# Kernel tuning notes

Measured on AMD Instinct MI355X. Metric: run time of the kernel, lower is better.

Reference implementation:

```python
import jax, jax.numpy as jnp
import numpy as np

B, N, M, C = 4, 4096, 4096, 256
IMG_W, IMG_H = 1280.0, 384.0


def setup_inputs() -> dict:
    key = jax.random.key(0)
    ks = jax.random.split(key, 12)
    nodes_L = jax.random.normal(ks[0], (B, N, C), dtype=jnp.float32)
    nodes_R = jax.random.normal(ks[1], (B, M, C), dtype=jnp.float32)
    # pixel coordinates: (u, v) with u in [0, IMG_W), v in [0, IMG_H)
    scale = jnp.array([IMG_W, IMG_H], dtype=jnp.float32)
    kpts_L = jax.random.uniform(ks[2], (B, N, 2), dtype=jnp.float32) * scale
    kpts_R = jax.random.uniform(ks[3], (B, M, 2), dtype=jnp.float32) * scale
    s = 1.0 / np.sqrt(C)
    Wq = jax.random.normal(ks[4], (C, C), dtype=jnp.float32) * s
    bq = jnp.zeros((C,), dtype=jnp.float32)
    Wk = jax.random.normal(ks[5], (C, C), dtype=jnp.float32) * s
    bk = jnp.zeros((C,), dtype=jnp.float32)
    Wv = jax.random.normal(ks[6], (C, C), dtype=jnp.float32) * s
    bv = jnp.zeros((C,), dtype=jnp.float32)
    Wm = jax.random.normal(ks[7], (C, C), dtype=jnp.float32) * s
    bm = jnp.zeros((C,), dtype=jnp.float32)
    return {"nodes_L": nodes_L, "nodes_R": nodes_R, "kpts_L": kpts_L, "kpts_R": kpts_R,
            "Wq": Wq, "bq": bq, "Wk": Wk, "bk": bk, "Wv": Wv, "bv": bv, "Wm": Wm, "bm": bm}


def reference(nodes_L, nodes_R, kpts_L, kpts_R, Wq, bq, Wk, bk, Wv, bv, Wm, bm):
    dim = nodes_L.shape[-1]
    # torch Linear: x @ W.T + b
    Q = nodes_L @ Wq.T + bq                      # [B,N,C]
    K = nodes_R @ Wk.T + bk                      # [B,M,C]
    V = nodes_R @ Wv.T + bv                      # [B,M,C]
    # epipolar geometry terms, [B,N,M]
    dist_v = jnp.abs(kpts_L[:, :, 1:2] - kpts_R[:, :, 1][:, None, :])
    dist_u = kpts_L[:, :, 0:1] - kpts_R[:, :, 0][:, None, :]
    mask = (dist_v < 3.0) & (dist_u > 0) & (dist_u < 192)
    attn = jnp.einsum('bnc,bmc->bnm', Q, K) / jnp.sqrt(jnp.float32(dim))
    attn = jnp.where(mask, attn, jnp.float32(-1e9))
    attn_weights = jax.nn.softmax(attn, axis=-1)  # [B,N,M]
    matched = jnp.einsum('bnm,bmc->bnc', attn_weights, V)
    init_disparity = jnp.sum(attn_weights * dist_u, axis=-1, keepdims=True)  # [B,N,1]
    confidence = jnp.any(mask, axis=-1, keepdims=True).astype(jnp.float32)   # [B,N,1]
    return matched @ Wm.T + bm, init_disparity, confidence
```

## Files before the change

### kernel.cpp

```cpp
#include <hip/hip_runtime.h>
#include <hip/hip_bf16.h>

#define BB 4
#define NN 4096
#define MM 4096
#define CC 256
#define CAP 128
#define NBIN 384
#define NCH 16
#define CHK 256

typedef __attribute__((ext_vector_type(8))) short bf16x8;
typedef __attribute__((ext_vector_type(4))) float f32x4;

static __device__ __forceinline__ float bf2f(unsigned short u) {
    return __uint_as_float(((unsigned)u) << 16);
}
static __device__ __forceinline__ unsigned short f2bf(float f) {
    unsigned u = __float_as_uint(f);
    u += 0x7fffu + ((u >> 16) & 1u);
    return (unsigned short)(u >> 16);
}
static __device__ __forceinline__ bf16x8 asbf(uint4 u) {
    union { uint4 a; bf16x8 b; } c; c.a = u; return c.b;
}
static __device__ __forceinline__ void gload16(const unsigned short* g, unsigned short* l) {
    __builtin_amdgcn_global_load_lds(
        (const __attribute__((address_space(1))) unsigned int*)g,
        (__attribute__((address_space(3))) unsigned int*)l, 16, 0, 0);
}

__global__ __launch_bounds__(256) void prep_kernel(
    const float* __restrict__ Wq, const float* __restrict__ Wk,
    const float* __restrict__ Wv, const float* __restrict__ Wm,
    const float* __restrict__ L, const float* __restrict__ R,
    const float* __restrict__ kptsR,
    unsigned short* __restrict__ Wpk, unsigned short* __restrict__ Lpk,
    unsigned short* __restrict__ Rpk,
    int* __restrict__ hist, unsigned short* __restrict__ prank,
    float* __restrict__ Vsum, float* __restrict__ Usum)
{
    __shared__ __align__(16) unsigned char SMEM[32768];
    const int tid = threadIdx.x, y = blockIdx.y, x = blockIdx.x;

    if (y < 4) {
        const float* S = (y == 0) ? Wq : (y == 1) ? Wk : (y == 2) ? Wv : Wm;
        int o = x * 256 + tid;
        int j = o & 7, lane = (o >> 3) & 63, kt = o >> 9;
        int kk = kt >> 4, t = kt & 15;
        int r = t * 16 + (lane & 15), c = kk * 32 + (lane >> 4) * 8 + j;
        Wpk[(size_t)y * 65536 + o] = f2bf(S[r * 256 + c]);
        return;
    }
    if (y < 6) {
        const float* S = (y == 5) ? R : L;
        unsigned short* D = (y == 5) ? Rpk : Lpk;
        unsigned short* T = (unsigned short*)SMEM;
        const int wid = tid >> 6, lane = tid & 63;
        const size_t R0 = (size_t)x * 64;
#pragma unroll
        for (int it = 0; it < 16; ++it) {
            int row = it * 4 + wid;
            float4 f = *(const float4*)(S + (R0 + row) * 256 + lane * 4);
            ushort4 h = make_ushort4(f2bf(f.x), f2bf(f.y), f2bf(f.z), f2bf(f.w));
            int col = lane * 4;
            *(ushort4*)&T[row * 256 + (col ^ ((row & 7) << 3))] = h;
        }
        __syncthreads();
        unsigned short* Dp = D + (size_t)x * 16384;
#pragma unroll
        for (int p = 0; p < 8; ++p) {
            int u = p * 2048 + tid * 8;
            int rt = u >> 12, rem = u & 4095;
            int kk = rem >> 9, ln = (rem >> 3) & 63;
            int row = rt * 16 + (ln & 15);
            int col = kk * 32 + (ln >> 4) * 8;
            *(uint4*)(Dp + u) = *(const uint4*)&T[row * 256 + (col ^ ((row & 7) << 3))];
        }
        return;
    }
    if (y == 6) {
        if (x >= NCH * BB) return;
        int chunk = x & 15, b = x >> 4;
        int* h = (int*)SMEM;
        short* sbin = (short*)(SMEM + NBIN * 4);
        for (int i = tid; i < NBIN; i += CHK) h[i] = 0;
        int m = chunk * CHK + tid;
        float2 p = ((const float2*)kptsR)[(size_t)b * MM + m];
        int bin = (int)p.y;
        sbin[tid] = (short)bin;
        __syncthreads();
        atomicAdd(&h[bin], 1);
        int r = 0;
        for (int t = 0; t < tid; ++t) r += (sbin[t] == bin);
        prank[(b << 12) + m] = (unsigned short)r;
        __syncthreads();
        for (int i = tid; i < NBIN; i += CHK)
            hist[((size_t)b * NCH + chunk) * NBIN + i] = h[i];
        return;
    }
    if (x < BB) {
        int b = x;
        float s = 0.f;
        for (int m = tid; m < MM; m += 256) s += kptsR[((size_t)b * MM + m) * 2 + 0];
#pragma unroll
        for (int off = 32; off; off >>= 1) s += __shfl_xor(s, off);
        float* sr = (float*)SMEM;
        int wave = tid >> 6, lane = tid & 63;
        if (lane == 0) sr[wave] = s;
        __syncthreads();
        if (tid == 0) Usum[b] = sr[0] + sr[1] + sr[2] + sr[3];
    } else if (x == BB) {
        for (int i = tid; i < BB * CC; i += 256) Vsum[i] = 0.f;
    }
}

template <bool OUT_BF16>
__global__ __launch_bounds__(256, 4) void proj_mfma_kernel(
    const unsigned short* __restrict__ A0, const unsigned short* __restrict__ A1,
    const unsigned short* __restrict__ A2, const unsigned short* __restrict__ Wpk,
    const float* __restrict__ b0, const float* __restrict__ b1, const float* __restrict__ b2,
    void* __restrict__ O0, void* __restrict__ O1, void* __restrict__ O2,
    float* __restrict__ Vsum,
    const int* __restrict__ hist, int* __restrict__ binStart, int* __restrict__ chunkOff)
{
    __shared__ __align__(16) unsigned char SMEM[32768];
    const int tid = threadIdx.x, wid = tid >> 6, lane = tid & 63;
    const int y = blockIdx.y;

    if (y == 3) {
        if (blockIdx.x >= BB) return;
        int b = blockIdx.x;
        int* sc = (int*)SMEM;
        for (int v = tid; v < NBIN; v += 256) {
            int tot = 0;
            for (int c = 0; c < NCH; ++c) tot += hist[((size_t)b * NCH + c) * NBIN + v];
            sc[v] = tot;
        }
        __syncthreads();
        for (int off = 1; off < NBIN; off <<= 1) {
            int v1 = tid + 256;
            int t0 = (tid >= off) ? sc[tid - off] : 0;
            int t1 = (v1 < NBIN && v1 >= off) ? sc[v1 - off] : 0;
            __syncthreads();
            sc[tid] += t0;
            if (v1 < NBIN) sc[v1] += t1;
            __syncthreads();
        }
        for (int v = tid; v < NBIN; v += 256) {
            int start = v ? sc[v - 1] : 0;
            binStart[b * (NBIN + 1) + v] = start;
            if (v == NBIN - 1) binStart[b * (NBIN + 1) + NBIN] = sc[NBIN - 1];
            int run = start;
            for (int c = 0; c < NCH; ++c) {
                chunkOff[((size_t)b * NCH + c) * NBIN + v] = run;
                run += hist[((size_t)b * NCH + c) * NBIN + v];
            }
        }
        return;
    }

    const int lrow = lane & 15, lk = lane >> 4;
    const unsigned short* A = (y == 0) ? A0 : (y == 1) ? A1 : A2;
    const float* bias = (y == 0) ? b0 : (y == 1) ? b1 : b2;
    void* Out = (y == 0) ? O0 : (y == 1) ? O1 : O2;
    const unsigned short* W = Wpk + (size_t)y * 65536;

    const int bid = blockIdx.x;
    const int g = (bid >> 3) & 3;
    const int rblk = (bid & 7) + ((bid >> 5) << 3);
    const size_t rbase = (size_t)rblk * 128;
    const int rt0 = rblk * 8 + wid * 2;

    unsigned short* Wl = (unsigned short*)SMEM;
#pragma unroll
    for (int i = 0; i < 8; ++i) {
        int kk = wid * 2 + (i >> 2), q = i & 3;
        gload16(W + (size_t)kk * 8192 + g * 2048 + q * 512 + lane * 8,
                Wl + kk * 2048 + q * 512 + lane * 8);
    }

    const unsigned short* Ap = A + (size_t)rt0 * 4096 + lane * 8;
    uint4 a[2][2];
    a[0][0] = *(const uint4*)(Ap);
    a[0][1] = *(const uint4*)(Ap + 4096);

    f32x4 acc[4][2];
#pragma unroll
    for (int t = 0; t < 4; ++t) {
        acc[t][0] = (f32x4){0.f, 0.f, 0.f, 0.f};
        acc[t][1] = (f32x4){0.f, 0.f, 0.f, 0.f};
    }

    asm volatile("s_waitcnt vmcnt(0)" ::: "memory");
    __syncthreads();

#pragma unroll
    for (int kk = 0; kk < 8; ++kk) {
        const int cur = kk & 1, nxt = cur ^ 1;
        if (kk < 7) {
            a[nxt][0] = *(const uint4*)(Ap + (kk + 1) * 512);
            a[nxt][1] = *(const uint4*)(Ap + 4096 + (kk + 1) * 512);
        }
        bf16x8 af0 = asbf(a[cur][0]);
        bf16x8 af1 = asbf(a[cur][1]);
#pragma unroll
        for (int t = 0; t < 4; ++t) {
            bf16x8 wf = *(const bf16x8*)(Wl + kk * 2048 + t * 512 + lane * 8);
            acc[t][0] = __builtin_amdgcn_mfma_f32_16x16x32_bf16(af0, wf, acc[t][0], 0, 0, 0);
            acc[t][1] = __builtin_amdgcn_mfma_f32_16x16x32_bf16(af1, wf, acc[t][1], 0, 0, 0);
        }
    }

    if (Vsum != nullptr && y == 2) {
#pragma unroll
        for (int t = 0; t < 4; ++t) {
            int col = g * 64 + t * 16 + lrow;
            float vs = acc[t][0][0] + acc[t][0][1] + acc[t][0][2] + acc[t][0][3]
                     + acc[t][1][0] + acc[t][1][1] + acc[t][1][2] + acc[t][1][3];
            vs += __shfl_xor(vs, 16);
            vs += __shfl_xor(vs, 32);
            if (lk == 0)
                atomicAdd(&Vsum[(rblk >> 5) * CC + col], vs + 32.f * bias[col]);
        }
    }

    __syncthreads();
    if constexpr (OUT_BF16) {
        unsigned short* Bo = (unsigned short*)SMEM;
#pragma unroll
        for (int t = 0; t < 4; ++t) {
            float bb = bias[g * 64 + t * 16 + lrow];
#pragma unroll
            for (int s = 0; s < 2; ++s)
#pragma unroll
                for (int rr = 0; rr < 4; ++rr) {
                    int row = wid * 32 + s * 16 + lk * 4 + rr;
                    Bo[row * 64 + t * 16 + lrow] = f2bf(acc[t][s][rr] + bb);
                }
        }
        __syncthreads();
        unsigned short* O = (unsigned short*)Out;
#pragma unroll
        for (int it = 0; it < 4; ++it) {
            int idx = it * 2048 + tid * 8;
            int row = idx >> 6, col = idx & 63;
            *(uint4*)(O + (rbase + row) * CC + g * 64 + col) = *(const uint4*)&Bo[idx];
        }
    } else {
        float* Bo = (float*)SMEM;
#pragma unroll
        for (int t = 0; t < 4; ++t) {
            float bb = bias[g * 64 + t * 16 + lrow];
#pragma unroll
            for (int s = 0; s < 2; ++s)
#pragma unroll
                for (int rr = 0; rr < 4; ++rr) {
                    int row = wid * 32 + s * 16 + lk * 4 + rr;
                    Bo[row * 64 + t * 16 + lrow] = acc[t][s][rr] + bb;
                }
        }
        __syncthreads();
        float* O = (float*)Out;
#pragma unroll
        for (int it = 0; it < 8; ++it) {
            int idx = it * 1024 + tid * 4;
            int row = idx >> 6, col = idx & 63;
            *(float4*)(O + (rbase + row) * CC + g * 64 + col) = *(const float4*)&Bo[idx];
        }
    }
}

__global__ __launch_bounds__(256) void bin_place_kernel(
    const float* __restrict__ kptsR, const int* __restrict__ chunkOff,
    const unsigned short* __restrict__ prank,
    unsigned short* __restrict__ sortedM, float2* __restrict__ sortedUV)
{
    int tid = threadIdx.x, chunk = blockIdx.x, b = blockIdx.y;
    int m = chunk * CHK + tid;
    float2 p = ((const float2*)kptsR)[(size_t)b * MM + m];
    int bin = (int)p.y;
    int pos = chunkOff[((size_t)b * NCH + chunk) * NBIN + bin] + prank[(b << 12) + m];
    sortedM[(b << 12) + pos] = (unsigned short)m;
    sortedUV[(b << 12) + pos] = p;
}

static __device__ __forceinline__ size_t mt_po(int bn, int lane) {
    return ((size_t)(bn >> 4)) * 4096 + (size_t)(lane >> 3) * 512
         + (size_t)(((lane >> 1) & 3) * 16 + (bn & 15)) * 8 + (lane & 1) * 4;
}

__global__ __launch_bounds__(256) void attn_kernel(
    const unsigned short* __restrict__ Q, const unsigned short* __restrict__ K,
    const unsigned short* __restrict__ V,
    const float* __restrict__ kptsL,
    const int* __restrict__ binStart, const unsigned short* __restrict__ sortedM,
    const float2* __restrict__ sortedUV,
    const float* __restrict__ Vsum, const float* __restrict__ Usum,
    unsigned short* __restrict__ Mpk, float* __restrict__ out1, float* __restrict__ out2)
{
    __shared__ unsigned short s_m[4][CAP];
    __shared__ float s_du[4][CAP];
    __shared__ float s_p[4][CAP];

    const int wid = threadIdx.x >> 6, lane = threadIdx.x & 63;
    const int bn = blockIdx.x * 4 + wid;
    const int b = bn >> 12;

    const int gi = lane >> 4, c = lane & 15;
    float qf[16];
    {
        const unsigned short* Qr = Q + (size_t)bn * CC + c * 16;
#pragma unroll
        for (int j = 0; j < 4; ++j) {
            ushort4 t = *(const ushort4*)(Qr + j * 4);
            qf[j * 4 + 0] = bf2f(t.x); qf[j * 4 + 1] = bf2f(t.y);
            qf[j * 4 + 2] = bf2f(t.z); qf[j * 4 + 3] = bf2f(t.w);
        }
    }

    float2 kl = *(const float2*)(kptsL + (size_t)bn * 2);
    float uL = kl.x, vL = kl.y;

    int ifl = (int)vL;
    int v0 = max(0, ifl - 3), v1 = min(NBIN - 1, ifl + 3);
    int s = binStart[b * (NBIN + 1) + v0];
    int e = binStart[b * (NBIN + 1) + v1 + 1];

    int cnt = 0;
    for (int i0 = s; i0 < e; i0 += 64) {
        int i = i0 + lane;
        bool valid = false;
        float du = 0.f;
        int m = 0;
        if (i < e) {
            float2 uv = sortedUV[(b << 12) + i];
            m = sortedM[(b << 12) + i];
            du = uL - uv.x;
            float dv = fabsf(vL - uv.y);
            valid = (dv < 3.0f) && (du > 0.0f) && (du < 192.0f);
        }
        unsigned long long bal = __ballot(valid);
        int pos = cnt + __popcll(bal & ((1ull << lane) - 1ull));
        if (valid && pos < CAP) { s_m[wid][pos] = (unsigned short)m; s_du[wid][pos] = du; }
        cnt += __popcll(bal);
    }
    if (cnt > CAP) cnt = CAP;

    if (cnt == 0) {
        float4 vs = *(const float4*)(Vsum + b * CC + lane * 4);
        ushort4 o = make_ushort4(f2bf(vs.x * (1.f / MM)), f2bf(vs.y * (1.f / MM)),
                                 f2bf(vs.z * (1.f / MM)), f2bf(vs.w * (1.f / MM)));
        *(ushort4*)(Mpk + mt_po(bn, lane)) = o;
        if (lane == 0) { out1[bn] = uL - Usum[b] * (1.f / MM); out2[bn] = 0.f; }
        return;
    }

    const unsigned short* Kb = K + (((size_t)b) << 12) * CC;
    for (int i0 = 0; i0 < cnt; i0 += 4) {
        int i = i0 + gi;
        int m = s_m[wid][(i < cnt) ? i : 0];
        const unsigned short* Kr = Kb + (size_t)m * CC + c * 16;
        float d = 0.f;
#pragma unroll
        for (int j = 0; j < 4; ++j) {
            ushort4 t = *(const ushort4*)(Kr + j * 4);
            d += qf[j * 4 + 0] * bf2f(t.x) + qf[j * 4 + 1] * bf2f(t.y)
               + qf[j * 4 + 2] * bf2f(t.z) + qf[j * 4 + 3] * bf2f(t.w);
        }
        d += __shfl_xor(d, 8); d += __shfl_xor(d, 4);
        d += __shfl_xor(d, 2); d += __shfl_xor(d, 1);
        if (c == 0 && i < cnt) s_p[wid][i] = d;
    }

    const float NEG = -3.0e38f;
    float mx, ps, ds, inv;
    if (cnt <= 64) {
        float x0 = (lane < cnt) ? s_p[wid][lane] * 0.0625f : NEG;
        mx = x0;
#pragma unroll
        for (int off = 32; off; off >>= 1) mx = fmaxf(mx, __shfl_xor(mx, off));
        float p0 = (lane < cnt) ? __expf(x0 - mx) : 0.f;
        float d0 = (lane < cnt) ? s_du[wid][lane] : 0.f;
        ps = p0; ds = p0 * d0;
#pragma unroll
        for (int off = 32; off; off >>= 1) { ps += __shfl_xor(ps, off); ds += __shfl_xor(ds, off); }
        inv = 1.f / ps;
        if (lane < cnt) s_p[wid][lane] = p0 * inv;
    } else {
        float x0 = (lane < cnt) ? s_p[wid][lane] * 0.0625f : NEG;
        float x1 = (lane + 64 < cnt) ? s_p[wid][lane + 64] * 0.0625f : NEG;
        mx = fmaxf(x0, x1);
#pragma unroll
        for (int off = 32; off; off >>= 1) mx = fmaxf(mx, __shfl_xor(mx, off));
        float p0 = (lane < cnt) ? __expf(x0 - mx) : 0.f;
        float p1 = (lane + 64 < cnt) ? __expf(x1 - mx) : 0.f;
        float d0 = (lane < cnt) ? s_du[wid][lane] : 0.f;
        float d1 = (lane + 64 < cnt) ? s_du[wid][lane + 64] : 0.f;
        ps = p0 + p1; ds = p0 * d0 + p1 * d1;
#pragma unroll
        for (int off = 32; off; off >>= 1) { ps += __shfl_xor(ps, off); ds += __shfl_xor(ds, off); }
        inv = 1.f / ps;
        if (lane < cnt) s_p[wid][lane] = p0 * inv;
        if (lane + 64 < cnt) s_p[wid][lane + 64] = p1 * inv;
    }

    const unsigned short* Vb = V + (((size_t)b) << 12) * CC;
    float a0 = 0.f, a1 = 0.f, a2 = 0.f, a3 = 0.f;
    float e0 = 0.f, e1 = 0.f, e2 = 0.f, e3 = 0.f;
    int i = 0;
    for (; i + 1 < cnt; i += 2) {
        float w0 = s_p[wid][i], w1 = s_p[wid][i + 1];
        ushort4 va = *(const ushort4*)(Vb + (size_t)s_m[wid][i] * CC + lane * 4);
        ushort4 vb = *(const ushort4*)(Vb + (size_t)s_m[wid][i + 1] * CC + lane * 4);
        a0 += w0 * bf2f(va.x); a1 += w0 * bf2f(va.y);
        a2 += w0 * bf2f(va.z); a3 += w0 * bf2f(va.w);
        e0 += w1 * bf2f(vb.x); e1 += w1 * bf2f(vb.y);
        e2 += w1 * bf2f(vb.z); e3 += w1 * bf2f(vb.w);
    }
    if (i < cnt) {
        float w0 = s_p[wid][i];
        ushort4 va = *(const ushort4*)(Vb + (size_t)s_m[wid][i] * CC + lane * 4);
        a0 += w0 * bf2f(va.x); a1 += w0 * bf2f(va.y);
        a2 += w0 * bf2f(va.z); a3 += w0 * bf2f(va.w);
    }
    ushort4 o = make_ushort4(f2bf(a0 + e0), f2bf(a1 + e1), f2bf(a2 + e2), f2bf(a3 + e3));
    *(ushort4*)(Mpk + mt_po(bn, lane)) = o;
    if (lane == 0) { out1[bn] = ds * inv; out2[bn] = 1.f; }
}

extern "C" void kernel_launch(void* const* d_in, const int* in_sizes, int n_in,
                              void* d_out, int out_size, void* d_ws, size_t ws_size,
                              hipStream_t stream) {
    const float* nodes_L = (const float*)d_in[0];
    const float* nodes_R = (const float*)d_in[1];
    const float* kpts_L  = (const float*)d_in[2];
    const float* kpts_R  = (const float*)d_in[3];
    const float* Wq = (const float*)d_in[4];
    const float* bq = (const float*)d_in[5];
    const float* Wk = (const float*)d_in[6];
    const float* bk = (const float*)d_in[7];
    const float* Wv = (const float*)d_in[8];
    const float* bv = (const float*)d_in[9];
    const float* Wm = (const float*)d_in[10];
    const float* bm = (const float*)d_in[11];

    char* ws = (char*)d_ws;
    unsigned short* Wpk = (unsigned short*)ws; ws += (size_t)4 * 65536 * 2;
    unsigned short* Lpk = (unsigned short*)ws; ws += (size_t)BB * NN * CC * 2;
    unsigned short* Rpk = (unsigned short*)ws; ws += (size_t)BB * MM * CC * 2;
    unsigned short* Qp  = (unsigned short*)ws; ws += (size_t)BB * NN * CC * 2;
    unsigned short* Kp  = (unsigned short*)ws; ws += (size_t)BB * MM * CC * 2;
    unsigned short* Vp  = (unsigned short*)ws; ws += (size_t)BB * MM * CC * 2;
    unsigned short* Mpk = (unsigned short*)ws; ws += (size_t)BB * NN * CC * 2;
    float* Vsum = (float*)ws;        ws += (size_t)BB * CC * 4;
    float* Usum = (float*)ws;        ws += (size_t)BB * 4;
    float2* sortedUV = (float2*)ws;  ws += (size_t)BB * MM * 8;
    int* binStart = (int*)ws;        ws += (size_t)BB * (NBIN + 1) * 4;
    unsigned short* sortedM = (unsigned short*)ws; ws += (size_t)BB * MM * 2;
    int* hist = (int*)ws;            ws += (size_t)BB * NCH * NBIN * 4;
    int* chunkOff = (int*)ws;        ws += (size_t)BB * NCH * NBIN * 4;
    unsigned short* prank = (unsigned short*)ws;

    float* out0 = (float*)d_out;
    float* out1 = out0 + (size_t)BB * NN * CC;
    float* out2 = out1 + (size_t)BB * NN;

    prep_kernel<<<dim3(256, 8), dim3(256), 0, stream>>>(
        Wq, Wk, Wv, Wm, nodes_L, nodes_R, kpts_R,
        Wpk, Lpk, Rpk, hist, prank, Vsum, Usum);

    proj_mfma_kernel<true><<<dim3(512, 4), dim3(256), 0, stream>>>(
        Lpk, Rpk, Rpk, Wpk, bq, bk, bv, Qp, Kp, Vp, Vsum,
        hist, binStart, chunkOff);

    bin_place_kernel<<<dim3(NCH, BB), dim3(256), 0, stream>>>(
        kpts_R, chunkOff, prank, sortedM, sortedUV);

    attn_kernel<<<dim3(BB * NN / 4), dim3(256), 0, stream>>>(
        Qp, Kp, Vp, kpts_L, binStart, sortedM, sortedUV, Vsum, Usum, Mpk, out1, out2);

    proj_mfma_kernel<false><<<dim3(512, 1), dim3(256), 0, stream>>>(
        Mpk, nullptr, nullptr, Wpk + 3 * 65536, bm, nullptr, nullptr,
        out0, nullptr, nullptr, nullptr, nullptr, nullptr, nullptr);
}
```

Measured before the change: 65.16 us.

## Fuse bin placement into scan blocks and output projection into attention

Folds the bin-placement kernel into the prefix-scan branch of the projection kernel, so each of 64 blocks computes its chunk offsets from a shared-memory copy of the histogram. The attention kernel now handles 16 queries per 1024-thread block, stages the matched rows in LDS and runs the Wm projection with MFMA in the same kernel. This drops two launches and the round trip of the intermediate matched tensor through global memory. In exchange, each block re-reads Wm from global memory, and the larger blocks with barriers may lower occupancy and let slow waves stall their block.

Measured after the change: 66.43 us. No clear change (+1.9%).

```diff
diff --git a/kernel.cpp b/kernel.cpp
--- a/kernel.cpp
+++ b/kernel.cpp
@@ -115,26 +115,32 @@
     }
 }
 
-template <bool OUT_BF16>
 __global__ __launch_bounds__(256, 4) void proj_mfma_kernel(
     const unsigned short* __restrict__ A0, const unsigned short* __restrict__ A1,
     const unsigned short* __restrict__ A2, const unsigned short* __restrict__ Wpk,
     const float* __restrict__ b0, const float* __restrict__ b1, const float* __restrict__ b2,
-    void* __restrict__ O0, void* __restrict__ O1, void* __restrict__ O2,
-    float* __restrict__ Vsum,
-    const int* __restrict__ hist, int* __restrict__ binStart, int* __restrict__ chunkOff)
+    unsigned short* __restrict__ O0, unsigned short* __restrict__ O1,
+    unsigned short* __restrict__ O2, float* __restrict__ Vsum,
+    const int* __restrict__ hist, int* __restrict__ binStart,
+    const float* __restrict__ kptsR, const unsigned short* __restrict__ prank,
+    unsigned short* __restrict__ sortedM, float2* __restrict__ sortedUV)
 {
     __shared__ __align__(16) unsigned char SMEM[32768];
     const int tid = threadIdx.x, wid = tid >> 6, lane = tid & 63;
     const int y = blockIdx.y;
 
     if (y == 3) {
-        if (blockIdx.x >= BB) return;
-        int b = blockIdx.x;
-        int* sc = (int*)SMEM;
+        if (blockIdx.x >= NCH * BB) return;
+        const int b = blockIdx.x >> 4, chunk = blockIdx.x & 15;
+        int* h2 = (int*)SMEM;
+        int* sc = (int*)(SMEM + 24576);
+        for (int i = tid; i < NCH * NBIN; i += 256)
+            h2[i] = hist[(size_t)b * NCH * NBIN + i];
+        __syncthreads();
         for (int v = tid; v < NBIN; v += 256) {
             int tot = 0;
-            for (int c = 0; c < NCH; ++c) tot += hist[((size_t)b * NCH + c) * NBIN + v];
+#pragma unroll
+            for (int c = 0; c < NCH; ++c) tot += h2[c * NBIN + v];
             sc[v] = tot;
         }
         __syncthreads();
@@ -147,23 +153,26 @@
             if (v1 < NBIN) sc[v1] += t1;
             __syncthreads();
         }
-        for (int v = tid; v < NBIN; v += 256) {
-            int start = v ? sc[v - 1] : 0;
-            binStart[b * (NBIN + 1) + v] = start;
-            if (v == NBIN - 1) binStart[b * (NBIN + 1) + NBIN] = sc[NBIN - 1];
-            int run = start;
-            for (int c = 0; c < NCH; ++c) {
-                chunkOff[((size_t)b * NCH + c) * NBIN + v] = run;
-                run += hist[((size_t)b * NCH + c) * NBIN + v];
-            }
-        }
+        if (chunk == 0) {
+            for (int v = tid; v < NBIN; v += 256)
+                binStart[b * (NBIN + 1) + v] = v ? sc[v - 1] : 0;
+            if (tid == 0) binStart[b * (NBIN + 1) + NBIN] = sc[NBIN - 1];
+        }
+        int m = chunk * CHK + tid;
+        float2 p = ((const float2*)kptsR)[(size_t)b * MM + m];
+        int bin = (int)p.y;
+        int ex = bin ? sc[bin - 1] : 0;
+        for (int c = 0; c < chunk; ++c) ex += h2[c * NBIN + bin];
+        int pos = ex + prank[(b << 12) + m];
+        sortedM[(b << 12) + pos] = (unsigned short)m;
+        sortedUV[(b << 12) + pos] = p;
         return;
     }
 
     const int lrow = lane & 15, lk = lane >> 4;
     const unsigned short* A = (y == 0) ? A0 : (y == 1) ? A1 : A2;
     const float* bias = (y == 0) ? b0 : (y == 1) ? b1 : b2;
-    void* Out = (y == 0) ? O0 : (y == 1) ? O1 : O2;
+    unsigned short* Out = (y == 0) ? O0 : (y == 1) ? O1 : O2;
     const unsigned short* W = Wpk + (size_t)y * 65536;
 
     const int bid = blockIdx.x;
@@ -226,85 +235,45 @@
     }
 
     __syncthreads();
-    if constexpr (OUT_BF16) {
-        unsigned short* Bo = (unsigned short*)SMEM;
-#pragma unroll
-        for (int t = 0; t < 4; ++t) {
-            float bb = bias[g * 64 + t * 16 + lrow];
-#pragma unroll
-            for (int s = 0; s < 2; ++s)
-#pragma unroll
-                for (int rr = 0; rr < 4; ++rr) {
-                    int row = wid * 32 + s * 16 + lk * 4 + rr;
-                    Bo[row * 64 + t * 16 + lrow] = f2bf(acc[t][s][rr] + bb);
-                }
-        }
-        __syncthreads();
-        unsigned short* O = (unsigned short*)Out;
-#pragma unroll
-        for (int it = 0; it < 4; ++it) {
-            int idx = it * 2048 + tid * 8;
-            int row = idx >> 6, col = idx & 63;
-            *(uint4*)(O + (rbase + row) * CC + g * 64 + col) = *(const uint4*)&Bo[idx];
-        }
-    } else {
-        float* Bo = (float*)SMEM;
-#pragma unroll
-        for (int t = 0; t < 4; ++t) {
-            float bb = bias[g * 64 + t * 16 + lrow];
-#pragma unroll
-            for (int s = 0; s < 2; ++s)
-#pragma unroll
-                for (int rr = 0; rr < 4; ++rr) {
-                    int row = wid * 32 + s * 16 + lk * 4 + rr;
-                    Bo[row * 64 + t * 16 + lrow] = acc[t][s][rr] + bb;
-                }
-        }
-        __syncthreads();
-        float* O = (float*)Out;
-#pragma unroll
-        for (int it = 0; it < 8; ++it) {
-            int idx = it * 1024 + tid * 4;
-            int row = idx >> 6, col = idx & 63;
-            *(float4*)(O + (rbase + row) * CC + g * 64 + col) = *(const float4*)&Bo[idx];
-        }
-    }
-}
-
-__global__ __launch_bounds__(256) void bin_place_kernel(
-    const float* __restrict__ kptsR, const int* __restrict__ chunkOff,
-    const unsigned short* __restrict__ prank,
-    unsigned short* __restrict__ sortedM, float2* __restrict__ sortedUV)
-{
-    int tid = threadIdx.x, chunk = blockIdx.x, b = blockIdx.y;
-    int m = chunk * CHK + tid;
-    float2 p = ((const float2*)kptsR)[(size_t)b * MM + m];
-    int bin = (int)p.y;
-    int pos = chunkOff[((size_t)b * NCH + chunk) * NBIN + bin] + prank[(b << 12) + m];
-    sortedM[(b << 12) + pos] = (unsigned short)m;
-    sortedUV[(b << 12) + pos] = p;
-}
-
-static __device__ __forceinline__ size_t mt_po(int bn, int lane) {
-    return ((size_t)(bn >> 4)) * 4096 + (size_t)(lane >> 3) * 512
-         + (size_t)(((lane >> 1) & 3) * 16 + (bn & 15)) * 8 + (lane & 1) * 4;
-}
-
-__global__ __launch_bounds__(256) void attn_kernel(
+    unsigned short* Bo = (unsigned short*)SMEM;
+#pragma unroll
+    for (int t = 0; t < 4; ++t) {
+        float bb = bias[g * 64 + t * 16 + lrow];
+#pragma unroll
+        for (int s = 0; s < 2; ++s)
+#pragma unroll
+            for (int rr = 0; rr < 4; ++rr) {
+                int row = wid * 32 + s * 16 + lk * 4 + rr;
+                Bo[row * 64 + t * 16 + lrow] = f2bf(acc[t][s][rr] + bb);
+            }
+    }
+    __syncthreads();
+#pragma unroll
+    for (int it = 0; it < 4; ++it) {
+        int idx = it * 2048 + tid * 8;
+        int row = idx >> 6, col = idx & 63;
+        *(uint4*)(Out + (rbase + row) * CC + g * 64 + col) = *(const uint4*)&Bo[idx];
+    }
+}
+
+__global__ __launch_bounds__(1024) void attn_out_kernel(
     const unsigned short* __restrict__ Q, const unsigned short* __restrict__ K,
     const unsigned short* __restrict__ V,
     const float* __restrict__ kptsL,
     const int* __restrict__ binStart, const unsigned short* __restrict__ sortedM,
     const float2* __restrict__ sortedUV,
     const float* __restrict__ Vsum, const float* __restrict__ Usum,
-    unsigned short* __restrict__ Mpk, float* __restrict__ out1, float* __restrict__ out2)
+    const unsigned short* __restrict__ Wmp, const float* __restrict__ bm,
+    float* __restrict__ out0, float* __restrict__ out1, float* __restrict__ out2)
 {
-    __shared__ unsigned short s_m[4][CAP];
-    __shared__ float s_du[4][CAP];
-    __shared__ float s_p[4][CAP];
+    __shared__ unsigned short s_m[16][CAP];
+    __shared__ float s_du[16][CAP];
+    __shared__ float s_p[16][CAP];
+    __shared__ __align__(16) unsigned short Mlds[16 * 256];
 
     const int wid = threadIdx.x >> 6, lane = threadIdx.x & 63;
-    const int bn = blockIdx.x * 4 + wid;
+    const int bn0 = blockIdx.x * 16;
+    const int bn = bn0 + wid;
     const int b = bn >> 12;
 
     const int gi = lane >> 4, c = lane & 15;
@@ -347,86 +316,103 @@
     }
     if (cnt > CAP) cnt = CAP;
 
+    const int mo = (lane >> 3) * 512 + (((lane >> 1) & 3) * 16 + wid) * 8 + (lane & 1) * 4;
+
     if (cnt == 0) {
         float4 vs = *(const float4*)(Vsum + b * CC + lane * 4);
         ushort4 o = make_ushort4(f2bf(vs.x * (1.f / MM)), f2bf(vs.y * (1.f / MM)),
                                  f2bf(vs.z * (1.f / MM)), f2bf(vs.w * (1.f / MM)));
-        *(ushort4*)(Mpk + mt_po(bn, lane)) = o;
+        *(ushort4*)&Mlds[mo] = o;
         if (lane == 0) { out1[bn] = uL - Usum[b] * (1.f / MM); out2[bn] = 0.f; }
-        return;
-    }
-
-    const unsigned short* Kb = K + (((size_t)b) << 12) * CC;
-    for (int i0 = 0; i0 < cnt; i0 += 4) {
-        int i = i0 + gi;
-        int m = s_m[wid][(i < cnt) ? i : 0];
-        const unsigned short* Kr = Kb + (size_t)m * CC + c * 16;
-        float d = 0.f;
-#pragma unroll
-        for (int j = 0; j < 4; ++j) {
-            ushort4 t = *(const ushort4*)(Kr + j * 4);
-            d += qf[j * 4 + 0] * bf2f(t.x) + qf[j * 4 + 1] * bf2f(t.y)
-               + qf[j * 4 + 2] * bf2f(t.z) + qf[j * 4 + 3] * bf2f(t.w);
-        }
-        d += __shfl_xor(d, 8); d += __shfl_xor(d, 4);
-        d += __shfl_xor(d, 2); d += __shfl_xor(d, 1);
-        if (c == 0 && i < cnt) s_p[wid][i] = d;
-    }
-
-    const float NEG = -3.0e38f;
-    float mx, ps, ds, inv;
-    if (cnt <= 64) {
-        float x0 = (lane < cnt) ? s_p[wid][lane] * 0.0625f : NEG;
-        mx = x0;
-#pragma unroll
-        for (int off = 32; off; off >>= 1) mx = fmaxf(mx, __shfl_xor(mx, off));
-        float p0 = (lane < cnt) ? __expf(x0 - mx) : 0.f;
-        float d0 = (lane < cnt) ? s_du[wid][lane] : 0.f;
-        ps = p0; ds = p0 * d0;
-#pragma unroll
-        for (int off = 32; off; off >>= 1) { ps += __shfl_xor(ps, off); ds += __shfl_xor(ds, off); }
-        inv = 1.f / ps;
-        if (lane < cnt) s_p[wid][lane] = p0 * inv;
     } else {
-        float x0 = (lane < cnt) ? s_p[wid][lane] * 0.0625f : NEG;
-        float x1 = (lane + 64 < cnt) ? s_p[wid][lane + 64] * 0.0625f : NEG;
-        mx = fmaxf(x0, x1);
-#pragma unroll
-        for (int off = 32; off; off >>= 1) mx = fmaxf(mx, __shfl_xor(mx, off));
-        float p0 = (lane < cnt) ? __expf(x0 - mx) : 0.f;
-        float p1 = (lane + 64 < cnt) ? __expf(x1 - mx) : 0.f;
-        float d0 = (lane < cnt) ? s_du[wid][lane] : 0.f;
-        float d1 = (lane + 64 < cnt) ? s_du[wid][lane + 64] : 0.f;
-        ps = p0 + p1; ds = p0 * d0 + p1 * d1;
-#pragma unroll
-        for (int off = 32; off; off >>= 1) { ps += __shfl_xor(ps, off); ds += __shfl_xor(ds, off); }
-        inv = 1.f / ps;
-        if (lane < cnt) s_p[wid][lane] = p0 * inv;
-        if (lane + 64 < cnt) s_p[wid][lane + 64] = p1 * inv;
-    }
-
-    const unsigned short* Vb = V + (((size_t)b) << 12) * CC;
-    float a0 = 0.f, a1 = 0.f, a2 = 0.f, a3 = 0.f;
-    float e0 = 0.f, e1 = 0.f, e2 = 0.f, e3 = 0.f;
-    int i = 0;
-    for (; i + 1 < cnt; i += 2) {
-        float w0 = s_p[wid][i], w1 = s_p[wid][i + 1];
-        ushort4 va = *(const ushort4*)(Vb + (size_t)s_m[wid][i] * CC + lane * 4);
-        ushort4 vb = *(const ushort4*)(Vb + (size_t)s_m[wid][i + 1] * CC + lane * 4);
-        a0 += w0 * bf2f(va.x); a1 += w0 * bf2f(va.y);
-        a2 += w0 * bf2f(va.z); a3 += w0 * bf2f(va.w);
-        e0 += w1 * bf2f(vb.x); e1 += w1 * bf2f(vb.y);
-        e2 += w1 * bf2f(vb.z); e3 += w1 * bf2f(vb.w);
-    }
-    if (i < cnt) {
-        float w0 = s_p[wid][i];
-        ushort4 va = *(const ushort4*)(Vb + (size_t)s_m[wid][i] * CC + lane * 4);
-        a0 += w0 * bf2f(va.x); a1 += w0 * bf2f(va.y);
-        a2 += w0 * bf2f(va.z); a3 += w0 * bf2f(va.w);
-    }
-    ushort4 o = make_ushort4(f2bf(a0 + e0), f2bf(a1 + e1), f2bf(a2 + e2), f2bf(a3 + e3));
-    *(ushort4*)(Mpk + mt_po(bn, lane)) = o;
-    if (lane == 0) { out1[bn] = ds * inv; out2[bn] = 1.f; }
+        const unsigned short* Kb = K + (((size_t)b) << 12) * CC;
+        for (int i0 = 0; i0 < cnt; i0 += 4) {
+            int i = i0 + gi;
+            int m = s_m[wid][(i < cnt) ? i : 0];
+            const unsigned short* Kr = Kb + (size_t)m * CC + c * 16;
+            float d = 0.f;
+#pragma unroll
+            for (int j = 0; j < 4; ++j) {
+                ushort4 t = *(const ushort4*)(Kr + j * 4);
+                d += qf[j * 4 + 0] * bf2f(t.x) + qf[j * 4 + 1] * bf2f(t.y)
+                   + qf[j * 4 + 2] * bf2f(t.z) + qf[j * 4 + 3] * bf2f(t.w);
+            }
+            d += __shfl_xor(d, 8); d += __shfl_xor(d, 4);
+            d += __shfl_xor(d, 2); d += __shfl_xor(d, 1);
+            if (c == 0 && i < cnt) s_p[wid][i] = d;
+        }
+
+        const float NEG = -3.0e38f;
+        float mx, ps, ds, inv;
+        if (cnt <= 64) {
+            float x0 = (lane < cnt) ? s_p[wid][lane] * 0.0625f : NEG;
+            mx = x0;
+#pragma unroll
+            for (int off = 32; off; off >>= 1) mx = fmaxf(mx, __shfl_xor(mx, off));
+            float p0 = (lane < cnt) ? __expf(x0 - mx) : 0.f;
+            float d0 = (lane < cnt) ? s_du[wid][lane] : 0.f;
+            ps = p0; ds = p0 * d0;
+#pragma unroll
+            for (int off = 32; off; off >>= 1) { ps += __shfl_xor(ps, off); ds += __shfl_xor(ds, off); }
+            inv = 1.f / ps;
+            if (lane < cnt) s_p[wid][lane] = p0 * inv;
+        } else {
+            float x0 = (lane < cnt) ? s_p[wid][lane] * 0.0625f : NEG;
+            float x1 = (lane + 64 < cnt) ? s_p[wid][lane + 64] * 0.0625f : NEG;
+            mx = fmaxf(x0, x1);
+#pragma unroll
+            for (int off = 32; off; off >>= 1) mx = fmaxf(mx, __shfl_xor(mx, off));
+            float p0 = (lane < cnt) ? __expf(x0 - mx) : 0.f;
+            float p1 = (lane + 64 < cnt) ? __expf(x1 - mx) : 0.f;
+            float d0 = (lane < cnt) ? s_du[wid][lane] : 0.f;
+            float d1 = (lane + 64 < cnt) ? s_du[wid][lane + 64] : 0.f;
+            ps = p0 + p1; ds = p0 * d0 + p1 * d1;
+#pragma unroll
+            for (int off = 32; off; off >>= 1) { ps += __shfl_xor(ps, off); ds += __shfl_xor(ds, off); }
+            inv = 1.f / ps;
+            if (lane < cnt) s_p[wid][lane] = p0 * inv;
+            if (lane + 64 < cnt) s_p[wid][lane + 64] = p1 * inv;
+        }
+
+        const unsigned short* Vb = V + (((size_t)b) << 12) * CC;
+        float a0 = 0.f, a1 = 0.f, a2 = 0.f, a3 = 0.f;
+        float e0 = 0.f, e1 = 0.f, e2 = 0.f, e3 = 0.f;
+        int i = 0;
+        for (; i + 1 < cnt; i += 2) {
+            float w0 = s_p[wid][i], w1 = s_p[wid][i + 1];
+            ushort4 va = *(const ushort4*)(Vb + (size_t)s_m[wid][i] * CC + lane * 4);
+            ushort4 vb = *(const ushort4*)(Vb + (size_t)s_m[wid][i + 1] * CC + lane * 4);
+            a0 += w0 * bf2f(va.x); a1 += w0 * bf2f(va.y);
+            a2 += w0 * bf2f(va.z); a3 += w0 * bf2f(va.w);
+            e0 += w1 * bf2f(vb.x); e1 += w1 * bf2f(vb.y);
+            e2 += w1 * bf2f(vb.z); e3 += w1 * bf2f(vb.w);
+        }
+        if (i < cnt) {
+            float w0 = s_p[wid][i];
+            ushort4 va = *(const ushort4*)(Vb + (size_t)s_m[wid][i] * CC + lane * 4);
+            a0 += w0 * bf2f(va.x); a1 += w0 * bf2f(va.y);
+            a2 += w0 * bf2f(va.z); a3 += w0 * bf2f(va.w);
+        }
+        ushort4 o = make_ushort4(f2bf(a0 + e0), f2bf(a1 + e1), f2bf(a2 + e2), f2bf(a3 + e3));
+        *(ushort4*)&Mlds[mo] = o;
+        if (lane == 0) { out1[bn] = ds * inv; out2[bn] = 1.f; }
+    }
+    __syncthreads();
+
+    f32x4 acc = (f32x4){0.f, 0.f, 0.f, 0.f};
+    const unsigned short* Wp = Wmp + wid * 512 + lane * 8;
+#pragma unroll
+    for (int kk = 0; kk < 8; ++kk) {
+        bf16x8 a = *(const bf16x8*)&Mlds[kk * 512 + lane * 8];
+        bf16x8 w = asbf(*(const uint4*)(Wp + (size_t)kk * 8192));
+        acc = __builtin_amdgcn_mfma_f32_16x16x32_bf16(a, w, acc, 0, 0, 0);
+    }
+    const int lrow = lane & 15, lk = lane >> 4;
+    int col = wid * 16 + lrow;
+    float bb = bm[col];
+#pragma unroll
+    for (int rr = 0; rr < 4; ++rr)
+        out0[(size_t)(bn0 + lk * 4 + rr) * CC + col] = acc[rr] + bb;
 }
 
 extern "C" void kernel_launch(void* const* d_in, const int* in_sizes, int n_in,
@@ -452,14 +438,12 @@
     unsigned short* Qp  = (unsigned short*)ws; ws += (size_t)BB * NN * CC * 2;
     unsigned short* Kp  = (unsigned short*)ws; ws += (size_t)BB * MM * CC * 2;
     unsigned short* Vp  = (unsigned short*)ws; ws += (size_t)BB * MM * CC * 2;
-    unsigned short* Mpk = (unsigned short*)ws; ws += (size_t)BB * NN * CC * 2;
     float* Vsum = (float*)ws;        ws += (size_t)BB * CC * 4;
     float* Usum = (float*)ws;        ws += (size_t)BB * 4;
     float2* sortedUV = (float2*)ws;  ws += (size_t)BB * MM * 8;
     int* binStart = (int*)ws;        ws += (size_t)BB * (NBIN + 1) * 4;
     unsigned short* sortedM = (unsigned short*)ws; ws += (size_t)BB * MM * 2;
     int* hist = (int*)ws;            ws += (size_t)BB * NCH * NBIN * 4;
-    int* chunkOff = (int*)ws;        ws += (size_t)BB * NCH * NBIN * 4;
     unsigned short* prank = (unsigned short*)ws;
 
     float* out0 = (float*)d_out;
@@ -470,17 +454,11 @@
         Wq, Wk, Wv, Wm, nodes_L, nodes_R, kpts_R,
         Wpk, Lpk, Rpk, hist, prank, Vsum, Usum);
 
-    proj_mfma_kernel<true><<<dim3(512, 4), dim3(256), 0, stream>>>(
+    proj_mfma_kernel<<<dim3(512, 4), dim3(256), 0, stream>>>(
         Lpk, Rpk, Rpk, Wpk, bq, bk, bv, Qp, Kp, Vp, Vsum,
-        hist, binStart, chunkOff);
-
-    bin_place_kernel<<<dim3(NCH, BB), dim3(256), 0, stream>>>(
-        kpts_R, chunkOff, prank, sortedM, sortedUV);
-
-    attn_kernel<<<dim3(BB * NN / 4), dim3(256), 0, stream>>>(
-        Qp, Kp, Vp, kpts_L, binStart, sortedM, sortedUV, Vsum, Usum, Mpk, out1, out2);
-
-    proj_mfma_kernel<false><<<dim3(512, 1), dim3(256), 0, stream>>>(
-        Mpk, nullptr, nullptr, Wpk + 3 * 65536, bm, nullptr, nullptr,
-        out0, nullptr, nullptr, nullptr, nullptr, nullptr, nullptr);
-}
+        hist, binStart, kpts_R, prank, sortedM, sortedUV);
+
+    attn_out_kernel<<<dim3(BB * NN / 16), dim3(1024), 0, stream>>>(
+        Qp, Kp, Vp, kpts_L, binStart, sortedM, sortedUV, Vsum, Usum,
+        Wpk + 3 * 65536, bm, out0, out1, out2);
+}
```
